# Optimization experiments

Measured on AMD Instinct MI355X. Metric: run time of the kernel, lower is better.

Reference implementation:

```python
import jax, jax.numpy as jnp
import numpy as np

N_POS = 2048
C_IN = 256
C_OUT = 256

def setup_inputs() -> dict:
    key = jax.random.key(0)
    k1, k2, k3 = jax.random.split(key, 3)
    x = jax.random.normal(k1, (64, C_IN, N_POS), dtype=jnp.float32)
    # Stacked per-position Conv1d(kernel=1) params: W[i] is [C_OUT, C_IN], b[i] is [C_OUT]
    bound = 1.0 / np.sqrt(C_IN)
    W = jax.random.uniform(k2, (N_POS, C_OUT, C_IN), jnp.float32, -bound, bound)
    b = jax.random.uniform(k3, (N_POS, C_OUT), jnp.float32, -bound, bound)
    return {"x": x, "W": W, "b": b}

def reference(x, W, b) -> jnp.ndarray:
    # Original: for each position i, out[:, :, i:i+1] = Conv1d_i(x[:, :, i:i+1])
    # = W[i] @ x[:, :, i] + b[i]. Fused as one batched GEMM over positions.
    out = jnp.einsum('bci,ioc->boi', x, W)  # [B, C_OUT, N_POS]
    return out + b.T[None, :, :]
```

## Files before the change

kernel.cpp:

```cpp
#include <hip/hip_runtime.h>


constexpr int NPOS = 2048;
constexpr int CIN  = 256;
constexpr int COUT = 256;
constexpr int NB   = 64;
constexpr int PP   = 2;
constexpr int XS_STRIDE = 264;
constexpr int NWG  = NPOS / PP;
constexpr int NXCD = 8;
constexpr int CPX  = NWG / NXCD;

typedef short short8 __attribute__((ext_vector_type(8)));
typedef float f32x4  __attribute__((ext_vector_type(4)));

__device__ __forceinline__ unsigned short f2bf(float f) {
  unsigned int u = __builtin_bit_cast(unsigned int, f);
  u += 0x7FFFu + ((u >> 16) & 1u);
  return (unsigned short)(u >> 16);
}

__global__ __launch_bounds__(256, 2)
void fc_kernel(const float* __restrict__ X, const float* __restrict__ W,
               const float* __restrict__ Bv, float* __restrict__ Out) {
  __shared__ __align__(16) unsigned short xs[PP * NB * XS_STRIDE];
  const int tid = threadIdx.x;

  const int bid = blockIdx.x;
  const int lb  = (bid & (NXCD - 1)) * CPX + (bid >> 3);
  const int i0  = lb * PP;

  {
    const int c = tid;
    #pragma unroll 4
    for (int b = 0; b < NB; ++b) {
      const float2 v = *(const float2*)(X + ((b * CIN + c) * NPOS + i0));
      xs[(0 * NB + b) * XS_STRIDE + c] = f2bf(v.x);
      xs[(1 * NB + b) * XS_STRIDE + c] = f2bf(v.y);
    }
  }
  __syncthreads();

  const int lane = tid & 63;
  const int wave = tid >> 6;
  const int lr = lane & 15;
  const int q  = lane >> 4;
  const int n0 = wave * 64;

  f32x4 acc[PP][4][4] = {};

  const float* W0 = W + (size_t)(i0 + 0) * (COUT * CIN);
  const float* W1 = W + (size_t)(i0 + 1) * (COUT * CIN);

  for (int k0 = 0; k0 < CIN; k0 += 32) {
    const int kk = k0 + q * 8;

    short8 a[PP][4];
    #pragma unroll
    for (int p = 0; p < PP; ++p)
      #pragma unroll
      for (int tm = 0; tm < 4; ++tm)
        a[p][tm] = *(const short8*)&xs[(p * NB + tm * 16 + lr) * XS_STRIDE + kk];

    #pragma unroll
    for (int p = 0; p < PP; ++p) {
      const float* Wi = (p == 0) ? W0 : W1;
      #pragma unroll
      for (int tn = 0; tn < 4; ++tn) {
        const float* wp = Wi + (n0 + tn * 16 + lr) * CIN + kk;
        const f32x4 w0 = __builtin_nontemporal_load((const f32x4*)wp);
        const f32x4 w1 = __builtin_nontemporal_load((const f32x4*)(wp + 4));
        short8 bb;
        bb[0] = (short)f2bf(w0[0]); bb[1] = (short)f2bf(w0[1]);
        bb[2] = (short)f2bf(w0[2]); bb[3] = (short)f2bf(w0[3]);
        bb[4] = (short)f2bf(w1[0]); bb[5] = (short)f2bf(w1[1]);
        bb[6] = (short)f2bf(w1[2]); bb[7] = (short)f2bf(w1[3]);
        #pragma unroll
        for (int tm = 0; tm < 4; ++tm)
          acc[p][tm][tn] = __builtin_amdgcn_mfma_f32_16x16x32_bf16(
              a[p][tm], bb, acc[p][tm][tn], 0, 0, 0);
      }
    }
  }

  #pragma unroll
  for (int tn = 0; tn < 4; ++tn) {
    const int o = n0 + tn * 16 + lr;
    const float bv0 = Bv[(i0 + 0) * COUT + o];
    const float bv1 = Bv[(i0 + 1) * COUT + o];
    #pragma unroll
    for (int tm = 0; tm < 4; ++tm) {
      #pragma unroll
      for (int r = 0; r < 4; ++r) {
        const int b = tm * 16 + q * 4 + r;
        float2 v;
        v.x = acc[0][tm][tn][r] + bv0;
        v.y = acc[1][tm][tn][r] + bv1;
        *(float2*)(Out + ((b * COUT + o) * NPOS + i0)) = v;
      }
    }
  }
}

extern "C" void kernel_launch(void* const* d_in, const int* in_sizes, int n_in,
                              void* d_out, int out_size, void* d_ws, size_t ws_size,
                              hipStream_t stream) {
  const float* X  = (const float*)d_in[0];
  const float* W  = (const float*)d_in[1];
  const float* Bv = (const float*)d_in[2];
  float* Out = (float*)d_out;
  dim3 grid(NWG);
  dim3 block(256);
  fc_kernel<<<grid, block, 0, stream>>>(X, W, Bv, Out);
}
```

Before: 1.005 ms.

## Retile work per block over 16 positions with N/M slicing for wider output stores

```diff
diff --git a/kernel.cpp b/kernel.cpp
--- a/kernel.cpp
+++ b/kernel.cpp
@@ -5,9 +5,11 @@
 constexpr int CIN  = 256;
 constexpr int COUT = 256;
 constexpr int NB   = 64;
-constexpr int PP   = 2;
+constexpr int IPC  = 16;
+constexpr int MH   = 32;
+constexpr int NC   = 64;
 constexpr int XS_STRIDE = 264;
-constexpr int NWG  = NPOS / PP;
+constexpr int NWG  = (NPOS/IPC) * (COUT/NC) * (NB/MH);
 constexpr int NXCD = 8;
 constexpr int CPX  = NWG / NXCD;
 
@@ -23,80 +25,89 @@
 __global__ __launch_bounds__(256, 2)
 void fc_kernel(const float* __restrict__ X, const float* __restrict__ W,
                const float* __restrict__ Bv, float* __restrict__ Out) {
-  __shared__ __align__(16) unsigned short xs[PP * NB * XS_STRIDE];
+  __shared__ __align__(16) unsigned short xs[2 * MH * XS_STRIDE];
+
   const int tid = threadIdx.x;
+  const int bid = blockIdx.x;
 
-  const int bid = blockIdx.x;
-  const int lb  = (bid & (NXCD - 1)) * CPX + (bid >> 3);
-  const int i0  = lb * PP;
-
-  {
-    const int c = tid;
-    #pragma unroll 4
-    for (int b = 0; b < NB; ++b) {
-      const float2 v = *(const float2*)(X + ((b * CIN + c) * NPOS + i0));
-      xs[(0 * NB + b) * XS_STRIDE + c] = f2bf(v.x);
-      xs[(1 * NB + b) * XS_STRIDE + c] = f2bf(v.y);
-    }
-  }
-  __syncthreads();
+  const int lb = (bid & (NXCD - 1)) * CPX + (bid >> 3);
+  const int chunk  = lb >> 3;
+  const int nslice = (lb >> 1) & 3;
+  const int mhalf  = lb & 1;
+  const int i0     = chunk * IPC;
+  const int m_base = mhalf * MH;
 
   const int lane = tid & 63;
   const int wave = tid >> 6;
   const int lr = lane & 15;
   const int q  = lane >> 4;
-  const int n0 = wave * 64;
+  const int n0 = nslice * NC + wave * 16;
+  const int o  = n0 + lr;
 
-  f32x4 acc[PP][4][4] = {};
+  f32x4 acc[IPC][2] = {};
 
-  const float* W0 = W + (size_t)(i0 + 0) * (COUT * CIN);
-  const float* W1 = W + (size_t)(i0 + 1) * (COUT * CIN);
+  #pragma unroll
+  for (int s = 0; s < IPC / 2; ++s) {
+    if (s) __syncthreads();
 
-  for (int k0 = 0; k0 < CIN; k0 += 32) {
-    const int kk = k0 + q * 8;
+    {
+      const int c = tid;
+      #pragma unroll 4
+      for (int bi = 0; bi < MH; ++bi) {
+        const float2 v = *(const float2*)(
+            X + ((size_t)((m_base + bi) * CIN + c)) * NPOS + i0 + 2 * s);
+        xs[(0 * MH + bi) * XS_STRIDE + c] = f2bf(v.x);
+        xs[(1 * MH + bi) * XS_STRIDE + c] = f2bf(v.y);
+      }
+    }
+    __syncthreads();
 
-    short8 a[PP][4];
-    #pragma unroll
-    for (int p = 0; p < PP; ++p)
-      #pragma unroll
-      for (int tm = 0; tm < 4; ++tm)
-        a[p][tm] = *(const short8*)&xs[(p * NB + tm * 16 + lr) * XS_STRIDE + kk];
+    const float* Wp0 = W + ((size_t)(i0 + 2 * s    ) * COUT + o) * CIN;
+    const float* Wp1 = W + ((size_t)(i0 + 2 * s + 1) * COUT + o) * CIN;
 
     #pragma unroll
-    for (int p = 0; p < PP; ++p) {
-      const float* Wi = (p == 0) ? W0 : W1;
+    for (int k0 = 0; k0 < CIN; k0 += 32) {
+      const int kk = k0 + q * 8;
       #pragma unroll
-      for (int tn = 0; tn < 4; ++tn) {
-        const float* wp = Wi + (n0 + tn * 16 + lr) * CIN + kk;
-        const f32x4 w0 = __builtin_nontemporal_load((const f32x4*)wp);
-        const f32x4 w1 = __builtin_nontemporal_load((const f32x4*)(wp + 4));
+      for (int p = 0; p < 2; ++p) {
+        const float* wp = (p ? Wp1 : Wp0) + kk;
+        const f32x4 w0 = *(const f32x4*)wp;
+        const f32x4 w1 = *(const f32x4*)(wp + 4);
         short8 bb;
         bb[0] = (short)f2bf(w0[0]); bb[1] = (short)f2bf(w0[1]);
         bb[2] = (short)f2bf(w0[2]); bb[3] = (short)f2bf(w0[3]);
         bb[4] = (short)f2bf(w1[0]); bb[5] = (short)f2bf(w1[1]);
         bb[6] = (short)f2bf(w1[2]); bb[7] = (short)f2bf(w1[3]);
         #pragma unroll
-        for (int tm = 0; tm < 4; ++tm)
-          acc[p][tm][tn] = __builtin_amdgcn_mfma_f32_16x16x32_bf16(
-              a[p][tm], bb, acc[p][tm][tn], 0, 0, 0);
+        for (int tm = 0; tm < 2; ++tm) {
+          const short8 a = *(const short8*)
+              &xs[(p * MH + tm * 16 + lr) * XS_STRIDE + kk];
+          acc[2 * s + p][tm] = __builtin_amdgcn_mfma_f32_16x16x32_bf16(
+              a, bb, acc[2 * s + p][tm], 0, 0, 0);
+        }
       }
     }
   }
 
+  float bv[IPC];
   #pragma unroll
-  for (int tn = 0; tn < 4; ++tn) {
-    const int o = n0 + tn * 16 + lr;
-    const float bv0 = Bv[(i0 + 0) * COUT + o];
-    const float bv1 = Bv[(i0 + 1) * COUT + o];
+  for (int ii = 0; ii < IPC; ++ii)
+    bv[ii] = Bv[(size_t)(i0 + ii) * COUT + o];
+
+  #pragma unroll
+  for (int tm = 0; tm < 2; ++tm) {
     #pragma unroll
-    for (int tm = 0; tm < 4; ++tm) {
+    for (int r = 0; r < 4; ++r) {
+      const int b = m_base + tm * 16 + q * 4 + r;
+      float* op = Out + ((size_t)(b * COUT + o)) * NPOS + i0;
       #pragma unroll
-      for (int r = 0; r < 4; ++r) {
-        const int b = tm * 16 + q * 4 + r;
-        float2 v;
-        v.x = acc[0][tm][tn][r] + bv0;
-        v.y = acc[1][tm][tn][r] + bv1;
-        *(float2*)(Out + ((b * COUT + o) * NPOS + i0)) = v;
+      for (int j = 0; j < 4; ++j) {
+        f32x4 v;
+        v[0] = acc[4 * j + 0][tm][r] + bv[4 * j + 0];
+        v[1] = acc[4 * j + 1][tm][r] + bv[4 * j + 1];
+        v[2] = acc[4 * j + 2][tm][r] + bv[4 * j + 2];
+        v[3] = acc[4 * j + 3][tm][r] + bv[4 * j + 3];
+        *(f32x4*)(op + 4 * j) = v;
       }
     }
   }
```

Result: slower. 1.193 ms (+18.7%).

## Pre-transpose X to bf16 in workspace and restructure GEMM into position chunks

Applied to the files above, without the earlier changes.

```diff
diff --git a/kernel.cpp b/kernel.cpp
--- a/kernel.cpp
+++ b/kernel.cpp
@@ -5,11 +5,10 @@
 constexpr int CIN  = 256;
 constexpr int COUT = 256;
 constexpr int NB   = 64;
-constexpr int PP   = 2;
-constexpr int XS_STRIDE = 264;
-constexpr int NWG  = NPOS / PP;
+constexpr int IPC  = 16;
+constexpr size_t XT_BYTES = (size_t)NPOS * NB * CIN * 2;
+
 constexpr int NXCD = 8;
-constexpr int CPX  = NWG / NXCD;
 
 typedef short short8 __attribute__((ext_vector_type(8)));
 typedef float f32x4  __attribute__((ext_vector_type(4)));
@@ -21,13 +20,130 @@
 }
 
 __global__ __launch_bounds__(256, 2)
-void fc_kernel(const float* __restrict__ X, const float* __restrict__ W,
-               const float* __restrict__ Bv, float* __restrict__ Out) {
+void xpose_kernel(const float* __restrict__ X, unsigned short* __restrict__ XT) {
+  __shared__ __align__(16) unsigned short tile[16 * 8 * 264];
+
+  const int tid = threadIdx.x;
+  const int bid = blockIdx.x;
+  const int it  = bid >> 3;
+  const int b0  = (bid & 7) * 8;
+  const int i0  = it * 16;
+
+  #pragma unroll
+  for (int k = 0; k < 8; ++k) {
+    const int b = b0 + k;
+    const int c = tid;
+    const float* p = X + ((size_t)(b * CIN + c)) * NPOS + i0;
+    const f32x4 v0 = *(const f32x4*)(p + 0);
+    const f32x4 v1 = *(const f32x4*)(p + 4);
+    const f32x4 v2 = *(const f32x4*)(p + 8);
+    const f32x4 v3 = *(const f32x4*)(p + 12);
+    #pragma unroll
+    for (int j = 0; j < 4; ++j) {
+      tile[((4 * 0 + j) * 8 + k) * 264 + c] = f2bf(v0[j]);
+      tile[((4 * 1 + j) * 8 + k) * 264 + c] = f2bf(v1[j]);
+      tile[((4 * 2 + j) * 8 + k) * 264 + c] = f2bf(v2[j]);
+      tile[((4 * 3 + j) * 8 + k) * 264 + c] = f2bf(v3[j]);
+    }
+  }
+  __syncthreads();
+
+  const int bp = tid >> 5;
+  const int c0 = (tid & 31) * 8;
+  #pragma unroll
+  for (int j = 0; j < 16; ++j) {
+    const short8 v = *(const short8*)&tile[(j * 8 + bp) * 264 + c0];
+    *(short8*)(XT + ((size_t)(i0 + j) * NB + b0 + bp) * CIN + c0) = v;
+  }
+}
+
+__global__ __launch_bounds__(256, 2)
+void fc_main(const unsigned short* __restrict__ XT, const float* __restrict__ W,
+             const float* __restrict__ Bv, float* __restrict__ Out) {
+  const int bid = blockIdx.x;
+  const int lb  = (bid & (NXCD - 1)) * 128 + (bid >> 3);
+  const int chunk = lb >> 3;
+  const int nsl   = lb & 7;
+  const int i0    = chunk * IPC;
+
+  const int tid  = threadIdx.x;
+  const int lane = tid & 63;
+  const int wave = tid >> 6;
+  const int lr = lane & 15;
+  const int q  = lane >> 4;
+  const int mh = wave >> 1;
+  const int nh = wave & 1;
+  const int m_base = mh * 32;
+  const int o  = nsl * 32 + nh * 16 + lr;
+
+  f32x4 acc[IPC][2] = {};
+
+  #pragma unroll
+  for (int s = 0; s < IPC / 2; ++s) {
+    const int ia = i0 + 2 * s;
+    const unsigned short* A0 = XT + ((size_t)(ia + 0) * NB + m_base) * CIN;
+    const unsigned short* A1 = XT + ((size_t)(ia + 1) * NB + m_base) * CIN;
+    const float* Wp0 = W + ((size_t)(ia + 0) * COUT + o) * CIN;
+    const float* Wp1 = W + ((size_t)(ia + 1) * COUT + o) * CIN;
+
+    #pragma unroll
+    for (int k0 = 0; k0 < CIN; k0 += 32) {
+      const int kk = k0 + q * 8;
+      #pragma unroll
+      for (int p = 0; p < 2; ++p) {
+        const float* wp = (p ? Wp1 : Wp0) + kk;
+        const f32x4 w0 = *(const f32x4*)wp;
+        const f32x4 w1 = *(const f32x4*)(wp + 4);
+        short8 bb;
+        bb[0] = (short)f2bf(w0[0]); bb[1] = (short)f2bf(w0[1]);
+        bb[2] = (short)f2bf(w0[2]); bb[3] = (short)f2bf(w0[3]);
+        bb[4] = (short)f2bf(w1[0]); bb[5] = (short)f2bf(w1[1]);
+        bb[6] = (short)f2bf(w1[2]); bb[7] = (short)f2bf(w1[3]);
+        const unsigned short* Ap = (p ? A1 : A0);
+        #pragma unroll
+        for (int tm = 0; tm < 2; ++tm) {
+          const short8 a = *(const short8*)(Ap + (tm * 16 + lr) * CIN + kk);
+          acc[2 * s + p][tm] = __builtin_amdgcn_mfma_f32_16x16x32_bf16(
+              a, bb, acc[2 * s + p][tm], 0, 0, 0);
+        }
+      }
+    }
+  }
+
+  float bv[IPC];
+  #pragma unroll
+  for (int ii = 0; ii < IPC; ++ii)
+    bv[ii] = Bv[(size_t)(i0 + ii) * COUT + o];
+
+  #pragma unroll
+  for (int tm = 0; tm < 2; ++tm) {
+    #pragma unroll
+    for (int r = 0; r < 4; ++r) {
+      const int b = m_base + tm * 16 + q * 4 + r;
+      float* op = Out + ((size_t)(b * COUT + o)) * NPOS + i0;
+      #pragma unroll
+      for (int j = 0; j < 4; ++j) {
+        f32x4 v;
+        v[0] = acc[4 * j + 0][tm][r] + bv[4 * j + 0];
+        v[1] = acc[4 * j + 1][tm][r] + bv[4 * j + 1];
+        v[2] = acc[4 * j + 2][tm][r] + bv[4 * j + 2];
+        v[3] = acc[4 * j + 3][tm][r] + bv[4 * j + 3];
+        *(f32x4*)(op + 4 * j) = v;
+      }
+    }
+  }
+}
+
+constexpr int PP = 2;
+constexpr int XS_STRIDE = 264;
+
+__global__ __launch_bounds__(256, 2)
+void fc_fallback(const float* __restrict__ X, const float* __restrict__ W,
+                 const float* __restrict__ Bv, float* __restrict__ Out) {
   __shared__ __align__(16) unsigned short xs[PP * NB * XS_STRIDE];
   const int tid = threadIdx.x;
-
   const int bid = blockIdx.x;
-  const int lb  = (bid & (NXCD - 1)) * CPX + (bid >> 3);
+  const int lb  = (bid & (NXCD - 1)) * 128 + (bid >> 3);
   const int i0  = lb * PP;
 
   {
@@ -48,13 +164,11 @@
   const int n0 = wave * 64;
 
   f32x4 acc[PP][4][4] = {};
-
   const float* W0 = W + (size_t)(i0 + 0) * (COUT * CIN);
   const float* W1 = W + (size_t)(i0 + 1) * (COUT * CIN);
 
   for (int k0 = 0; k0 < CIN; k0 += 32) {
     const int kk = k0 + q * 8;
-
     short8 a[PP][4];
     #pragma unroll
     for (int p = 0; p < PP; ++p)
@@ -68,8 +182,8 @@
       #pragma unroll
       for (int tn = 0; tn < 4; ++tn) {
         const float* wp = Wi + (n0 + tn * 16 + lr) * CIN + kk;
-        const f32x4 w0 = __builtin_nontemporal_load((const f32x4*)wp);
-        const f32x4 w1 = __builtin_nontemporal_load((const f32x4*)(wp + 4));
+        const f32x4 w0 = *(const f32x4*)wp;
+        const f32x4 w1 = *(const f32x4*)(wp + 4);
         short8 bb;
         bb[0] = (short)f2bf(w0[0]); bb[1] = (short)f2bf(w0[1]);
         bb[2] = (short)f2bf(w0[2]); bb[3] = (short)f2bf(w0[3]);
@@ -109,7 +223,12 @@
   const float* W  = (const float*)d_in[1];
   const float* Bv = (const float*)d_in[2];
   float* Out = (float*)d_out;
-  dim3 grid(NWG);
-  dim3 block(256);
-  fc_kernel<<<grid, block, 0, stream>>>(X, W, Bv, Out);
-}
+
+  if (d_ws != nullptr && ws_size >= XT_BYTES) {
+    unsigned short* XT = (unsigned short*)d_ws;
+    xpose_kernel<<<dim3(128 * 8), dim3(256), 0, stream>>>(X, XT);
+    fc_main<<<dim3(1024), dim3(256), 0, stream>>>(XT, W, Bv, Out);
+  } else {
+    fc_fallback<<<dim3(1024), dim3(256), 0, stream>>>(X, W, Bv, Out);
+  }
+}
```

After: 1.046 ms. +4.1%, slower.
